# Performance work log

Hardware: AMD Instinct MI355X
Metric: run time of the kernel (lower is better)

## Reference

```python
import jax, jax.numpy as jnp
import numpy as np

N_NODES = 100000
N_EDGES = 1600000
K = 5  # TAGConv hops
F_IN, F_HID, F_OUT = 64, 128, 64


def setup_inputs() -> dict:
    key = jax.random.key(0)
    ks = jax.random.split(key, 6)
    x = jax.random.normal(ks[0], (N_NODES, F_IN), dtype=jnp.float32)
    edge_index = jax.random.randint(ks[1], (2, N_EDGES), 0, N_NODES, dtype=jnp.int32)
    edge_weight = jax.random.uniform(ks[2], (N_EDGES,), dtype=jnp.float32)
    # TAGConv layer l has (K+1) weight matrices stacked as [K+1, in, out] + one bias
    W0 = jax.random.normal(ks[3], (K + 1, F_IN, F_HID), dtype=jnp.float32) * 0.05
    b0 = jnp.zeros((F_HID,), dtype=jnp.float32)
    W1 = jax.random.normal(ks[4], (K + 1, F_HID, F_OUT), dtype=jnp.float32) * 0.05
    b1 = jnp.zeros((F_OUT,), dtype=jnp.float32)
    return {"x": x, "edge_index": edge_index, "edge_weight": edge_weight,
            "W0": W0, "b0": b0, "W1": W1, "b1": b1}


def _gcn_norm(edge_weight, row, col):
    # symmetric normalization, no added self-loops (TAGConv default with edge_weight)
    deg = jax.ops.segment_sum(edge_weight, col, num_segments=N_NODES)
    safe_deg = jnp.where(deg > 0, deg, 1.0)
    dis = jnp.where(deg > 0, jax.lax.rsqrt(safe_deg), 0.0)  # deg^-1/2, 0 for isolated
    return dis[row] * edge_weight * dis[col]


def _tag_conv(x, row, col, norm, W, b):
    # out = sum_{k=0..K} (A_norm^k x) @ W[k] + b
    out = x @ W[0]
    h = x
    for k in range(1, K + 1):
        msg = h[row] * norm[:, None]                    # gather + scale  [E, F]
        h = jax.ops.segment_sum(msg, col, num_segments=N_NODES)  # scatter-add [N, F]
        out = out + h @ W[k]
    return out + b


def reference(x, edge_index, edge_weight, W0, b0, W1, b1):
    row, col = edge_index[0], edge_index[1]
    norm = _gcn_norm(edge_weight, row, col)
    h = jax.nn.leaky_relu(_tag_conv(x, row, col, norm, W0, b0), negative_slope=0.01)
    h = jax.nn.leaky_relu(_tag_conv(h, row, col, norm, W1, b1), negative_slope=0.01)
    return h
```

## Files before the change

### kernel.cpp

```cpp
#include <hip/hip_runtime.h>


namespace {
constexpr int NN = 100000;
constexpr int NE = 1600000;
constexpr int TPB = 256;

typedef __attribute__((ext_vector_type(8))) short short8v;
typedef __attribute__((ext_vector_type(4))) float float4v;

__device__ __forceinline__ float bflo(unsigned p) { return __uint_as_float(p << 16); }
__device__ __forceinline__ float bfhi(unsigned p) { return __uint_as_float(p & 0xffff0000u); }
__device__ __forceinline__ unsigned f2bf(float x) {
  unsigned u = __float_as_uint(x);
  return (u + 0x7fffu + ((u >> 16) & 1u)) >> 16;
}
__device__ __forceinline__ unsigned pack2(float lo, float hi) {
  return f2bf(lo) | (f2bf(hi) << 16);
}

__global__ void pass1_kernel(const int* __restrict__ col, const float* __restrict__ w,
                             unsigned long long* __restrict__ acc64, int* __restrict__ rank) {
  int e0 = blockIdx.x * (TPB * 2) + threadIdx.x;
  int e1 = e0 + TPB;
  int c0 = col[e0], c1 = col[e1];
  unsigned long long v0 = (1ULL << 40) | (unsigned long long)__float2uint_rn(w[e0] * 16777216.0f);
  unsigned long long v1 = (1ULL << 40) | (unsigned long long)__float2uint_rn(w[e1] * 16777216.0f);
  unsigned long long o0 = atomicAdd(&acc64[c0], v0);
  unsigned long long o1 = atomicAdd(&acc64[c1], v1);
  rank[e0] = (int)(o0 >> 40);
  rank[e1] = (int)(o1 >> 40);
}

__global__ void dis_kernel(const unsigned long long* __restrict__ acc64,
                           float* __restrict__ dis) {
  int n = blockIdx.x * TPB + threadIdx.x;
  if (n >= NN) return;
  unsigned long long u = acc64[n] & ((1ULL << 40) - 1);
  float d = (float)u * (1.0f / 16777216.0f);
  dis[n] = d > 0.f ? rsqrtf(d) : 0.f;
}

__global__ void scan1_kernel(const unsigned long long* __restrict__ acc64,
                             int* __restrict__ excl, int* __restrict__ btot) {
  __shared__ int sh[1024];
  int i = blockIdx.x * 1024 + threadIdx.x;
  int v = (i < NN) ? (int)(acc64[i] >> 40) : 0;
  sh[threadIdx.x] = v;
  __syncthreads();
  for (int ofs = 1; ofs < 1024; ofs <<= 1) {
    int t = (threadIdx.x >= ofs) ? sh[threadIdx.x - ofs] : 0;
    __syncthreads();
    sh[threadIdx.x] += t;
    __syncthreads();
  }
  if (i < NN) excl[i] = sh[threadIdx.x] - v;
  if (threadIdx.x == 1023) btot[blockIdx.x] = sh[1023];
}

__global__ void scan2_kernel(int* __restrict__ btot, int nb) {
  __shared__ int sh[128];
  int t = threadIdx.x;
  if (t < nb) sh[t] = btot[t];
  __syncthreads();
  if (t == 0) {
    int run = 0;
    for (int b = 0; b < nb; ++b) { int x = sh[b]; sh[b] = run; run += x; }
  }
  __syncthreads();
  if (t < nb) btot[t] = sh[t];
}

__global__ void scan3_kernel(const int* __restrict__ excl, const int* __restrict__ btot,
                             int* __restrict__ rowptr) {
  int i = blockIdx.x * TPB + threadIdx.x;
  if (i < NN) rowptr[i] = excl[i] + btot[i >> 10];
  if (i == NN) rowptr[NN] = NE;
}

__global__ void fill2_kernel(const int* __restrict__ row, const int* __restrict__ col,
                             const float* __restrict__ w, const float* __restrict__ dis,
                             const int* __restrict__ rank, const int* __restrict__ rowptr,
                             int2* __restrict__ edges) {
  int e = blockIdx.x * TPB + threadIdx.x;
  if (e >= NE) return;
  int r = row[e], c = col[e];
  float nw = dis[r] * w[e] * dis[c];
  edges[rowptr[c] + rank[e]] = make_int2(r, __float_as_int(nw));
}

__global__ void wfrag0_kernel(const float* __restrict__ W0, short* __restrict__ F) {
  int t = blockIdx.x * TPB + threadIdx.x;
  if (t >= 12 * 8 * 64) return;
  int l = t & 63, nt = (t >> 6) & 7, s = t >> 9;
  int c = nt * 16 + (l & 15);
  int kb = s * 32 + (l >> 4) * 8;
  short8v v;
#pragma unroll
  for (int j = 0; j < 8; ++j) v[j] = (short)f2bf(W0[(kb + j) * 128 + c]);
  *(short8v*)(F + (size_t)t * 8) = v;
}

__global__ void wfrag1_kernel(const float* __restrict__ W1, short* __restrict__ F) {
  int t = blockIdx.x * TPB + threadIdx.x;
  if (t >= 4 * 24 * 64) return;
  int l = t & 63, nt = (t >> 6) % 24, s = t / (64 * 24);
  int J = nt * 16 + (l & 15);
  int fb = s * 32 + (l >> 4) * 8;
  const float* Wb = W1 + (size_t)(J >> 6) * (128 * 64) + (J & 63);
  short8v v;
#pragma unroll
  for (int j = 0; j < 8; ++j) v[j] = (short)f2bf(Wb[(size_t)(fb + j) * 64]);
  *(short8v*)(F + (size_t)t * 8) = v;
}

__global__ void convx_kernel(const float* __restrict__ x, unsigned* __restrict__ hcat) {
  unsigned idx = blockIdx.x * (unsigned)TPB + threadIdx.x;
  if (idx >= (unsigned)NN * 32u) return;
  unsigned n = idx >> 5, p = idx & 31u;
  float2 v = *(const float2*)(x + (size_t)n * 64 + p * 2);
  hcat[(size_t)n * 192 + p] = pack2(v.x, v.y);
}

__device__ __forceinline__ void fma8(float* a, uint4 p, float w) {
  a[0] = fmaf(bflo(p.x), w, a[0]); a[1] = fmaf(bfhi(p.x), w, a[1]);
  a[2] = fmaf(bflo(p.y), w, a[2]); a[3] = fmaf(bfhi(p.y), w, a[3]);
  a[4] = fmaf(bflo(p.z), w, a[4]); a[5] = fmaf(bfhi(p.z), w, a[5]);
  a[6] = fmaf(bflo(p.w), w, a[6]); a[7] = fmaf(bfhi(p.w), w, a[7]);
}

template <bool YADD, bool FINAL>
__global__ void hop_kernel(const unsigned short* __restrict__ src, int sstride,
                           const int2* __restrict__ edges, const int* __restrict__ rowptr,
                           const unsigned short* __restrict__ y,
                           unsigned short* __restrict__ dst, int dstride,
                           const float* __restrict__ bias, float* __restrict__ outf) {
  unsigned n = blockIdx.x * 32u + (threadIdx.x >> 3);
  unsigned lane = threadIdx.x & 7u;
  unsigned f0 = lane * 8u;
  int e = rowptr[n], e1 = rowptr[n + 1];
  float a[8] = {};
  for (; e + 3 < e1; e += 4) {
    int2 d0 = edges[e], d1 = edges[e + 1], d2 = edges[e + 2], d3 = edges[e + 3];
    uint4 p0 = *(const uint4*)(src + (size_t)(unsigned)d0.x * sstride + f0);
    uint4 p1 = *(const uint4*)(src + (size_t)(unsigned)d1.x * sstride + f0);
    uint4 p2 = *(const uint4*)(src + (size_t)(unsigned)d2.x * sstride + f0);
    uint4 p3 = *(const uint4*)(src + (size_t)(unsigned)d3.x * sstride + f0);
    fma8(a, p0, __int_as_float(d0.y));
    fma8(a, p1, __int_as_float(d1.y));
    fma8(a, p2, __int_as_float(d2.y));
    fma8(a, p3, __int_as_float(d3.y));
  }
  if (e + 1 < e1) {
    int2 d0 = edges[e], d1 = edges[e + 1];
    uint4 p0 = *(const uint4*)(src + (size_t)(unsigned)d0.x * sstride + f0);
    uint4 p1 = *(const uint4*)(src + (size_t)(unsigned)d1.x * sstride + f0);
    fma8(a, p0, __int_as_float(d0.y));
    fma8(a, p1, __int_as_float(d1.y));
    e += 2;
  }
  if (e < e1) {
    int2 d0 = edges[e];
    uint4 p0 = *(const uint4*)(src + (size_t)(unsigned)d0.x * sstride + f0);
    fma8(a, p0, __int_as_float(d0.y));
  }
  if (YADD) {
    uint4 yv = *(const uint4*)(y + (size_t)n * 384 + f0);
    a[0] += bflo(yv.x); a[1] += bfhi(yv.x);
    a[2] += bflo(yv.y); a[3] += bfhi(yv.y);
    a[4] += bflo(yv.z); a[5] += bfhi(yv.z);
    a[6] += bflo(yv.w); a[7] += bfhi(yv.w);
  }
  if (FINAL) {
    const float4* bp = (const float4*)(bias + f0);
    float4 bv0 = bp[0], bv1 = bp[1];
    float4 o0, o1;
    o0.x = a[0] + bv0.x; o0.y = a[1] + bv0.y; o0.z = a[2] + bv0.z; o0.w = a[3] + bv0.w;
    o1.x = a[4] + bv1.x; o1.y = a[5] + bv1.y; o1.z = a[6] + bv1.z; o1.w = a[7] + bv1.w;
    o0.x = o0.x >= 0.f ? o0.x : 0.01f * o0.x; o0.y = o0.y >= 0.f ? o0.y : 0.01f * o0.y;
    o0.z = o0.z >= 0.f ? o0.z : 0.01f * o0.z; o0.w = o0.w >= 0.f ? o0.w : 0.01f * o0.w;
    o1.x = o1.x >= 0.f ? o1.x : 0.01f * o1.x; o1.y = o1.y >= 0.f ? o1.y : 0.01f * o1.y;
    o1.z = o1.z >= 0.f ? o1.z : 0.01f * o1.z; o1.w = o1.w >= 0.f ? o1.w : 0.01f * o1.w;
    float4* op = (float4*)(outf + (size_t)n * 64 + f0);
    op[0] = o0; op[1] = o1;
  } else {
    uint4 st;
    st.x = pack2(a[0], a[1]); st.y = pack2(a[2], a[3]);
    st.z = pack2(a[4], a[5]); st.w = pack2(a[6], a[7]);
    *(uint4*)(dst + (size_t)n * dstride + f0) = st;
  }
}

__global__ void gemm_l0(const unsigned short* __restrict__ A, const short* __restrict__ W0f,
                        const float* __restrict__ bias, unsigned short* __restrict__ H1) {
  int wave = threadIdx.x >> 6, lane = threadIdx.x & 63;
  int lrow = lane & 15, lk = lane >> 4;
  unsigned r0 = blockIdx.x * 64u + (unsigned)wave * 16u;
  unsigned arow = r0 + (unsigned)lrow;
  if (arow >= NN) arow = NN - 1;
  const short8v* Ab = (const short8v*)(A + (size_t)arow * 384 + (unsigned)lk * 8);
  const short8v* Bb = (const short8v*)W0f + lane;
  float4v acc[8] = {};
#pragma unroll
  for (int s = 0; s < 12; ++s) {
    short8v a = Ab[s * 4];
#pragma unroll
    for (int nt = 0; nt < 8; ++nt) {
      short8v b = Bb[(s * 8 + nt) * 64];
      acc[nt] = __builtin_amdgcn_mfma_f32_16x16x32_bf16(a, b, acc[nt], 0, 0, 0);
    }
  }
#pragma unroll
  for (int nt = 0; nt < 8; ++nt) {
    int c = nt * 16 + lrow;
    float bv = bias[c];
#pragma unroll
    for (int r = 0; r < 4; ++r) {
      unsigned n = r0 + (unsigned)(lk * 4 + r);
      if (n < NN) {
        float v = acc[nt][r] + bv;
        v = v >= 0.f ? v : 0.01f * v;
        H1[(size_t)n * 128 + c] = (unsigned short)f2bf(v);
      }
    }
  }
}

__global__ void gemm_l1(const unsigned short* __restrict__ A, const short* __restrict__ W1f,
                        unsigned short* __restrict__ Y) {
  int wave = threadIdx.x >> 6, lane = threadIdx.x & 63;
  int lrow = lane & 15, lk = lane >> 4;
  int yb = blockIdx.y * 8;
  unsigned r0 = blockIdx.x * 64u + (unsigned)wave * 16u;
  unsigned arow = r0 + (unsigned)lrow;
  if (arow >= NN) arow = NN - 1;
  const short8v* Ab = (const short8v*)(A + (size_t)arow * 128 + (unsigned)lk * 8);
  const short8v* Bb = (const short8v*)W1f + lane;
  float4v acc[8] = {};
#pragma unroll
  for (int s = 0; s < 4; ++s) {
    short8v a = Ab[s * 4];
#pragma unroll
    for (int nt = 0; nt < 8; ++nt) {
      short8v b = Bb[(s * 24 + yb + nt) * 64];
      acc[nt] = __builtin_amdgcn_mfma_f32_16x16x32_bf16(a, b, acc[nt], 0, 0, 0);
    }
  }
#pragma unroll
  for (int nt = 0; nt < 8; ++nt) {
    int c = (yb + nt) * 16 + lrow;
#pragma unroll
    for (int r = 0; r < 4; ++r) {
      unsigned n = r0 + (unsigned)(lk * 4 + r);
      if (n < NN) Y[(size_t)n * 384 + c] = (unsigned short)f2bf(acc[nt][r]);
    }
  }
}

}

extern "C" void kernel_launch(void* const* d_in, const int* in_sizes, int n_in,
                              void* d_out, int out_size, void* d_ws, size_t ws_size,
                              hipStream_t stream) {
  const float* x  = (const float*)d_in[0];
  const int*   ei = (const int*)d_in[1];
  const float* ew = (const float*)d_in[2];
  const float* W0 = (const float*)d_in[3];
  const float* b0 = (const float*)d_in[4];
  const float* W1 = (const float*)d_in[5];
  const float* b1 = (const float*)d_in[6];
  float* out = (float*)d_out;
  const int* row = ei;
  const int* col = ei + NE;

  constexpr size_t OFF_DIS    = 0;
  constexpr size_t OFF_ROWPTR = 100352;
  constexpr size_t OFF_BTOT   = OFF_ROWPTR + 100352;
  constexpr size_t OFF_EDGES  = OFF_BTOT + 128;
  constexpr size_t OFF_HCAT   = OFF_EDGES + 2 * (size_t)NE;
  constexpr size_t OFF_H1     = OFF_HCAT + (size_t)NN * 384 / 2;
  constexpr size_t WS_WORDS   = OFF_H1 + (size_t)NN * 128 / 2;
  if (ws_size < WS_WORDS * sizeof(float)) return;

  float* ws = (float*)d_ws;
  float* dis    = ws + OFF_DIS;
  int*   rowptr = (int*)(ws + OFF_ROWPTR);
  int*   btot   = (int*)(ws + OFF_BTOT);
  int2*  edges  = (int2*)(ws + OFF_EDGES);
  unsigned short* Hcat = (unsigned short*)(ws + OFF_HCAT);
  unsigned short* H1   = (unsigned short*)(ws + OFF_H1);
  short* W0f = (short*)(ws + OFF_DIS);
  short* W1f = (short*)(ws + OFF_DIS + 24576);
  unsigned long long* acc64 = (unsigned long long*)(ws + OFF_H1);
  int* excl = (int*)(ws + OFF_H1 + 200704);
  int* rank = (int*)Hcat;
  unsigned short* z0 = H1;
  unsigned short* z1 = H1 + (size_t)NN * 64;

  hipMemsetAsync(acc64, 0, NN * sizeof(unsigned long long), stream);
  pass1_kernel<<<NE / (TPB * 2), TPB, 0, stream>>>(col, ew, acc64, rank);
  dis_kernel<<<(NN + TPB - 1) / TPB, TPB, 0, stream>>>(acc64, dis);
  scan1_kernel<<<98, 1024, 0, stream>>>(acc64, excl, btot);
  scan2_kernel<<<1, 128, 0, stream>>>(btot, 98);
  scan3_kernel<<<(NN + TPB) / TPB, TPB, 0, stream>>>(excl, btot, rowptr);
  fill2_kernel<<<(NE + TPB - 1) / TPB, TPB, 0, stream>>>(row, col, ew, dis, rank, rowptr, edges);
  wfrag0_kernel<<<24, TPB, 0, stream>>>(W0, W0f);
  wfrag1_kernel<<<24, TPB, 0, stream>>>(W1, W1f);

  convx_kernel<<<NN * 32 / TPB, TPB, 0, stream>>>(x, (unsigned*)Hcat);
  for (int k = 1; k <= 5; ++k) {
    hop_kernel<false, false><<<NN / 32, TPB, 0, stream>>>(
        Hcat + (k - 1) * 64, 384, edges, rowptr, nullptr,
        Hcat + k * 64, 384, nullptr, nullptr);
  }
  gemm_l0<<<(NN + 63) / 64, TPB, 0, stream>>>(Hcat, W0f, b0, H1);

  gemm_l1<<<dim3((NN + 63) / 64, 3), TPB, 0, stream>>>(H1, W1f, Hcat);
  const unsigned short* Y = Hcat;
  hop_kernel<true, false><<<NN / 32, TPB, 0, stream>>>(
      Y + 5 * 64, 384, edges, rowptr, Y + 4 * 64, z0, 64, nullptr, nullptr);
  hop_kernel<true, false><<<NN / 32, TPB, 0, stream>>>(
      z0, 64, edges, rowptr, Y + 3 * 64, z1, 64, nullptr, nullptr);
  hop_kernel<true, false><<<NN / 32, TPB, 0, stream>>>(
      z1, 64, edges, rowptr, Y + 2 * 64, z0, 64, nullptr, nullptr);
  hop_kernel<true, false><<<NN / 32, TPB, 0, stream>>>(
      z0, 64, edges, rowptr, Y + 1 * 64, z1, 64, nullptr, nullptr);
  hop_kernel<true, true><<<NN / 32, TPB, 0, stream>>>(
      z1, 64, edges, rowptr, Y + 0 * 64, nullptr, 0, b1, out);
}
```

Baseline: 620.8 us.

## Sort nodes by degree into virtual segments for load-balanced hop kernels

```diff
diff --git a/kernel.cpp b/kernel.cpp
--- a/kernel.cpp
+++ b/kernel.cpp
@@ -21,15 +21,18 @@
 
 __global__ void pass1_kernel(const int* __restrict__ col, const float* __restrict__ w,
                              unsigned long long* __restrict__ acc64, int* __restrict__ rank) {
-  int e0 = blockIdx.x * (TPB * 2) + threadIdx.x;
-  int e1 = e0 + TPB;
-  int c0 = col[e0], c1 = col[e1];
-  unsigned long long v0 = (1ULL << 40) | (unsigned long long)__float2uint_rn(w[e0] * 16777216.0f);
-  unsigned long long v1 = (1ULL << 40) | (unsigned long long)__float2uint_rn(w[e1] * 16777216.0f);
-  unsigned long long o0 = atomicAdd(&acc64[c0], v0);
-  unsigned long long o1 = atomicAdd(&acc64[c1], v1);
-  rank[e0] = (int)(o0 >> 40);
-  rank[e1] = (int)(o1 >> 40);
+  int base = blockIdx.x * (TPB * 4) + threadIdx.x;
+#pragma unroll
+  for (int i = 0; i < 4; ++i) {
+    int e = base + i * TPB;
+    if (e < NE) {
+      int c = col[e];
+      unsigned long long v =
+          (1ULL << 40) | (unsigned long long)__float2uint_rn(w[e] * 16777216.0f);
+      unsigned long long old = atomicAdd(&acc64[c], v);
+      rank[e] = (int)(old >> 40);
+    }
+  }
 }
 
 __global__ void dis_kernel(const unsigned long long* __restrict__ acc64,
@@ -89,6 +92,48 @@
   edges[rowptr[c] + rank[e]] = make_int2(r, __float_as_int(nw));
 }
 
+__global__ void dhist_kernel(const int* __restrict__ rowptr, int* __restrict__ ghist) {
+  __shared__ int lh[128];
+  if (threadIdx.x < 128) lh[threadIdx.x] = 0;
+  __syncthreads();
+  int n = blockIdx.x * TPB + threadIdx.x;
+  if (n < NN) {
+    int d = rowptr[n + 1] - rowptr[n];
+    atomicAdd(&lh[min(d, 127)], 1);
+  }
+  __syncthreads();
+  if (threadIdx.x < 128 && lh[threadIdx.x]) atomicAdd(&ghist[threadIdx.x], lh[threadIdx.x]);
+}
+
+__global__ void dscan_kernel(const int* __restrict__ ghist, int* __restrict__ gcur) {
+  if (threadIdx.x == 0) {
+    int run = 0;
+    for (int b = 127; b >= 0; --b) { gcur[b] = run; run += ghist[b]; }
+  }
+}
+
+__global__ void dscatter_kernel(const int* __restrict__ rowptr, int* __restrict__ gcur,
+                                int4* __restrict__ vseg) {
+  __shared__ int lh[128], lbase[128], lcur[128];
+  if (threadIdx.x < 128) { lh[threadIdx.x] = 0; lcur[threadIdx.x] = 0; }
+  __syncthreads();
+  int n = blockIdx.x * TPB + threadIdx.x;
+  int e0 = 0, e1 = 0, bin = 0;
+  if (n < NN) {
+    e0 = rowptr[n]; e1 = rowptr[n + 1];
+    bin = min(e1 - e0, 127);
+    atomicAdd(&lh[bin], 1);
+  }
+  __syncthreads();
+  if (threadIdx.x < 128)
+    lbase[threadIdx.x] = lh[threadIdx.x] ? atomicAdd(&gcur[threadIdx.x], lh[threadIdx.x]) : 0;
+  __syncthreads();
+  if (n < NN) {
+    int off = atomicAdd(&lcur[bin], 1);
+    vseg[lbase[bin] + off] = make_int4(e0, e1, n, 0);
+  }
+}
+
 __global__ void wfrag0_kernel(const float* __restrict__ W0, short* __restrict__ F) {
   int t = blockIdx.x * TPB + threadIdx.x;
   if (t >= 12 * 8 * 64) return;
@@ -129,16 +174,25 @@
   a[6] = fmaf(bflo(p.w), w, a[6]); a[7] = fmaf(bfhi(p.w), w, a[7]);
 }
 
-template <bool YADD, bool FINAL>
+template <bool VSEG, bool YADD, bool FINAL>
 __global__ void hop_kernel(const unsigned short* __restrict__ src, int sstride,
                            const int2* __restrict__ edges, const int* __restrict__ rowptr,
+                           const int4* __restrict__ vseg,
                            const unsigned short* __restrict__ y,
                            unsigned short* __restrict__ dst, int dstride,
                            const float* __restrict__ bias, float* __restrict__ outf) {
-  unsigned n = blockIdx.x * 32u + (threadIdx.x >> 3);
+  unsigned vn = blockIdx.x * 32u + (threadIdx.x >> 3);
   unsigned lane = threadIdx.x & 7u;
   unsigned f0 = lane * 8u;
-  int e = rowptr[n], e1 = rowptr[n + 1];
+  int e, e1;
+  unsigned n;
+  if (VSEG) {
+    int4 s = vseg[vn];
+    e = s.x; e1 = s.y; n = (unsigned)s.z;
+  } else {
+    n = vn;
+    e = rowptr[n]; e1 = rowptr[n + 1];
+  }
   float a[8] = {};
   for (; e + 3 < e1; e += 4) {
     int2 d0 = edges[e], d1 = edges[e + 1], d2 = edges[e + 2], d3 = edges[e + 3];
@@ -296,35 +350,42 @@
   int* rank = (int*)Hcat;
   unsigned short* z0 = H1;
   unsigned short* z1 = H1 + (size_t)NN * 64;
+  int4* vseg = (int4*)d_out;
+  int* ghist = (int*)d_out + 400000;
+  int* gcur  = ghist + 128;
 
   hipMemsetAsync(acc64, 0, NN * sizeof(unsigned long long), stream);
-  pass1_kernel<<<NE / (TPB * 2), TPB, 0, stream>>>(col, ew, acc64, rank);
+  hipMemsetAsync(ghist, 0, 256 * sizeof(int), stream);
+  pass1_kernel<<<(NE + TPB * 4 - 1) / (TPB * 4), TPB, 0, stream>>>(col, ew, acc64, rank);
   dis_kernel<<<(NN + TPB - 1) / TPB, TPB, 0, stream>>>(acc64, dis);
   scan1_kernel<<<98, 1024, 0, stream>>>(acc64, excl, btot);
   scan2_kernel<<<1, 128, 0, stream>>>(btot, 98);
   scan3_kernel<<<(NN + TPB) / TPB, TPB, 0, stream>>>(excl, btot, rowptr);
   fill2_kernel<<<(NE + TPB - 1) / TPB, TPB, 0, stream>>>(row, col, ew, dis, rank, rowptr, edges);
+  dhist_kernel<<<(NN + TPB - 1) / TPB, TPB, 0, stream>>>(rowptr, ghist);
+  dscan_kernel<<<1, 64, 0, stream>>>(ghist, gcur);
+  dscatter_kernel<<<(NN + TPB - 1) / TPB, TPB, 0, stream>>>(rowptr, gcur, vseg);
   wfrag0_kernel<<<24, TPB, 0, stream>>>(W0, W0f);
   wfrag1_kernel<<<24, TPB, 0, stream>>>(W1, W1f);
 
   convx_kernel<<<NN * 32 / TPB, TPB, 0, stream>>>(x, (unsigned*)Hcat);
   for (int k = 1; k <= 5; ++k) {
-    hop_kernel<false, false><<<NN / 32, TPB, 0, stream>>>(
-        Hcat + (k - 1) * 64, 384, edges, rowptr, nullptr,
+    hop_kernel<true, false, false><<<NN / 32, TPB, 0, stream>>>(
+        Hcat + (k - 1) * 64, 384, edges, rowptr, vseg, nullptr,
         Hcat + k * 64, 384, nullptr, nullptr);
   }
   gemm_l0<<<(NN + 63) / 64, TPB, 0, stream>>>(Hcat, W0f, b0, H1);
 
   gemm_l1<<<dim3((NN + 63) / 64, 3), TPB, 0, stream>>>(H1, W1f, Hcat);
   const unsigned short* Y = Hcat;
-  hop_kernel<true, false><<<NN / 32, TPB, 0, stream>>>(
-      Y + 5 * 64, 384, edges, rowptr, Y + 4 * 64, z0, 64, nullptr, nullptr);
-  hop_kernel<true, false><<<NN / 32, TPB, 0, stream>>>(
-      z0, 64, edges, rowptr, Y + 3 * 64, z1, 64, nullptr, nullptr);
-  hop_kernel<true, false><<<NN / 32, TPB, 0, stream>>>(
-      z1, 64, edges, rowptr, Y + 2 * 64, z0, 64, nullptr, nullptr);
-  hop_kernel<true, false><<<NN / 32, TPB, 0, stream>>>(
-      z0, 64, edges, rowptr, Y + 1 * 64, z1, 64, nullptr, nullptr);
-  hop_kernel<true, true><<<NN / 32, TPB, 0, stream>>>(
-      z1, 64, edges, rowptr, Y + 0 * 64, nullptr, 0, b1, out);
-}
+  hop_kernel<true, true, false><<<NN / 32, TPB, 0, stream>>>(
+      Y + 5 * 64, 384, edges, rowptr, vseg, Y + 4 * 64, z0, 64, nullptr, nullptr);
+  hop_kernel<true, true, false><<<NN / 32, TPB, 0, stream>>>(
+      z0, 64, edges, rowptr, vseg, Y + 3 * 64, z1, 64, nullptr, nullptr);
+  hop_kernel<true, true, false><<<NN / 32, TPB, 0, stream>>>(
+      z1, 64, edges, rowptr, vseg, Y + 2 * 64, z0, 64, nullptr, nullptr);
+  hop_kernel<true, true, false><<<NN / 32, TPB, 0, stream>>>(
+      z0, 64, edges, rowptr, vseg, Y + 1 * 64, z1, 64, nullptr, nullptr);
+  hop_kernel<false, true, true><<<NN / 32, TPB, 0, stream>>>(
+      z1, 64, edges, rowptr, nullptr, Y + 0 * 64, nullptr, 0, b1, out);
+}
```

Result: slower. 640.1 us (+3.1%).
